# Performance work log

Measured on AMD Instinct MI355X. Metric: run time of the kernel, lower is better.

Reference implementation:

```python
import jax, jax.numpy as jnp
import numpy as np
import math

F_DIM = 256      # feature_dims
NHEADS = 4
KEY_D = 64
VAL_D = 64
ITERS = 6        # update_iters
N_ATOMS = 100000
N_BONDS = 200000
NEI = 6
ATOM_FDIM = 31
BOND_FDIM = 37   # 31 + 6
NEG_SLOPE = 0.1


def setup_inputs() -> dict:
    key = jax.random.key(0)
    ks = jax.random.split(key, 13)
    s = 0.05
    return {
        "fatoms": jax.random.normal(ks[0], (N_ATOMS, ATOM_FDIM), jnp.float32),
        "fbonds": jax.random.normal(ks[1], (N_BONDS, BOND_FDIM), jnp.float32),
        "agraph": jax.random.randint(ks[2], (N_ATOMS, NEI), 0, N_BONDS),
        "bgraph": jax.random.randint(ks[3], (N_BONDS, NEI), 0, N_BONDS),
        "lig_scope": jax.random.randint(ks[4], (64, 2), 0, N_ATOMS),
        "W_emb": jax.random.normal(ks[5], (BOND_FDIM, F_DIM), jnp.float32) * s,
        "b_emb": jnp.zeros((F_DIM,), jnp.float32),
        "Wq": jax.random.normal(ks[6], (F_DIM, NHEADS * KEY_D), jnp.float32) * s,
        "Wk": jax.random.normal(ks[7], (F_DIM, NHEADS * KEY_D), jnp.float32) * s,
        "Wv": jax.random.normal(ks[8], (F_DIM, NHEADS * VAL_D), jnp.float32) * s,
        "Wout": jax.random.normal(ks[9], (VAL_D, F_DIM), jnp.float32) * s,
        "W_last": jax.random.normal(ks[10], (ATOM_FDIM + F_DIM, F_DIM), jnp.float32) * s,
        "b_last": jnp.zeros((F_DIM,), jnp.float32),
    }


def reference(fatoms, fbonds, agraph, bgraph, lig_scope,
              W_emb, b_emb, Wq, Wk, Wv, Wout, W_last, b_last):
    # Bond embedding + initial message
    fbonds_input = fbonds @ W_emb + b_emb                      # [B, F]
    message = jax.nn.leaky_relu(fbonds_input, NEG_SLOPE)
    # index 0 is the padding bond -> masked out in attention
    nei_mask = jnp.where(bgraph != 0, 0.0, -1e7)[:, None, :]   # [B, 1, NEI]
    inv_sqrt_kd = 1.0 / math.sqrt(KEY_D)

    for _ in range(ITERS - 1):
        nei = message[bgraph]                                  # [B, NEI, F] gather
        q = (message @ Wq).reshape(N_BONDS, NHEADS, KEY_D)     # [B, H, K]
        k = (nei @ Wk).reshape(N_BONDS, NEI, NHEADS, KEY_D)    # [B, NEI, H, K]
        v = (nei @ Wv).reshape(N_BONDS, NEI, NHEADS, VAL_D)    # [B, NEI, H, V]
        scores = jnp.einsum('bhk,bnhk->bhn', q, k) * inv_sqrt_kd + nei_mask
        attn = jax.nn.softmax(scores, axis=-1)                 # [B, H, NEI]
        out = jnp.einsum('bhn,bnhv->bhv', attn, v)             # [B, H, V]
        out = out.mean(axis=1)                                 # mean over heads -> [B, V]
        message = jax.nn.leaky_relu(fbonds_input + out @ Wout, NEG_SLOPE)

    # Aggregate incoming bond messages per atom (index 0 acts as padding row)
    nei_sum = message[agraph].sum(axis=1)                      # [A, F]
    h = jnp.concatenate([fatoms, nei_sum], axis=-1) @ W_last + b_last
    return jax.nn.leaky_relu(h, NEG_SLOPE)
```

## Files before the change

kernel.cpp:

```cpp
#include <hip/hip_runtime.h>

#define N_ATOMS 100000
#define N_BONDS 200000
#define NEI 6
#define ITERS 6

#define MB_PAD 200064
#define MT_B 1563
#define MT_A 782
#define KL 320
#define KVSTRIDE 768
#define QSTR 260

typedef __bf16 bf16x8 __attribute__((ext_vector_type(8)));
typedef float f32x4 __attribute__((ext_vector_type(4)));

__device__ __forceinline__ float b2f(unsigned short u) {
  union { unsigned int i; float f; } x; x.i = ((unsigned int)u) << 16; return x.f;
}
__device__ __forceinline__ unsigned short f2b(float f) {
  union { float f; unsigned int i; } x; x.f = f;
  unsigned int r = (x.i + 0x7FFFu + ((x.i >> 16) & 1u)) >> 16;
  return (unsigned short)r;
}
__device__ __forceinline__ float lrelu(float v) { return v > 0.f ? v : 0.1f * v; }

#if defined(__has_builtin)
#  if __has_builtin(__builtin_amdgcn_cvt_f32_fp8) && __has_builtin(__builtin_amdgcn_cvt_pk_fp8_f32)
#    define HW_FP8 1
#  endif
#endif

__device__ __forceinline__ unsigned char f2e4m3_sw(float f) {
  union { float f; unsigned u; } x; x.f = f;
  unsigned s = (x.u >> 24) & 0x80u;
  unsigned ax = x.u & 0x7FFFFFFFu;
  if (ax >= 0x43E00000u) return (unsigned char)(s | 0x7Eu);
  if (ax < 0x3A800000u)  return (unsigned char)s;
  if (ax < 0x3C800000u) {
    union { unsigned u; float f; } a; a.u = ax;
    unsigned n = (unsigned)(a.f * 512.0f + 0.5f);
    return (unsigned char)(s | n);
  }
  unsigned r = ax + 0x0007FFFFu + ((ax >> 20) & 1u);
  unsigned e32 = r >> 23;
  unsigned mant = (r >> 20) & 7u;
  int e8 = (int)e32 - 120;
  if (e8 >= 16) return (unsigned char)(s | 0x7Eu);
  return (unsigned char)(s | ((unsigned)e8 << 3) | mant);
}
__device__ __forceinline__ float dec8_sw(unsigned b) {
  unsigned s = (b & 0x80u) << 24;
  unsigned e = (b >> 3) & 0xFu, m = b & 7u;
  if (e) { union { unsigned u; float f; } x; x.u = s | ((e + 120u) << 23) | (m << 20); return x.f; }
  float v = (float)m * 0.001953125f;
  return (b & 0x80u) ? -v : v;
}
#ifdef HW_FP8
__device__ __forceinline__ unsigned char f2e4m3(float f) {
  return (unsigned char)(__builtin_amdgcn_cvt_pk_fp8_f32(f, f, 0, false) & 0xFF);
}
#define DEC0(x) __builtin_amdgcn_cvt_f32_fp8((int)(x), 0)
#define DEC1(x) __builtin_amdgcn_cvt_f32_fp8((int)(x), 1)
#define DEC2(x) __builtin_amdgcn_cvt_f32_fp8((int)(x), 2)
#define DEC3(x) __builtin_amdgcn_cvt_f32_fp8((int)(x), 3)
#else
__device__ __forceinline__ unsigned char f2e4m3(float f) { return f2e4m3_sw(f); }
#define DEC0(x) dec8_sw((x) & 0xFFu)
#define DEC1(x) dec8_sw(((x) >> 8) & 0xFFu)
#define DEC2(x) dec8_sw(((x) >> 16) & 0xFFu)
#define DEC3(x) dec8_sw(((x) >> 24) & 0xFFu)
#endif

__global__ __launch_bounds__(256) void pack_weights(
    const float* __restrict__ Wq, const float* __restrict__ Wk,
    const float* __restrict__ Wv, const float* __restrict__ Wemb,
    const float* __restrict__ Wout, const float* __restrict__ Wlast,
    unsigned short* __restrict__ wkvT, unsigned short* __restrict__ wqT,
    unsigned short* __restrict__ wmsgT, unsigned short* __restrict__ wlastT)
{
  int t = blockIdx.x * 256 + threadIdx.x;
  {
    int n = t >> 8, k = t & 255;
    wkvT[t] = f2b((n < 256) ? Wk[k * 256 + n] : Wv[k * 256 + (n - 256)]);
  }
  if (t < 65536) {
    int n = t >> 8, k = t & 255;
    wqT[t] = f2b(Wq[k * 256 + n]);
  }
  if (t < 32768) {
    int n = t >> 7, k = t & 127;
    float v = 0.f;
    if (k < 64)       v = Wout[k * 256 + n];
    else if (k < 101) v = Wemb[(k - 64) * 256 + n];
    wmsgT[t] = f2b(v);
  }
  if (t < 256 * KL) {
    int n = t / KL, k = t % KL;
    float v = 0.f;
    if (k < 256)      v = Wlast[(31 + k) * 256 + n];
    else if (k < 287) v = Wlast[(k - 256) * 256 + n];
    wlastT[t] = f2b(v);
  }
}

__global__ __launch_bounds__(256) void pack_bonds(
    const float* __restrict__ fbonds, unsigned short* __restrict__ A2)
{
  int t = blockIdx.x * 256 + threadIdx.x;
  int r = t >> 7, c = t & 127;
  float v = 0.f;
  if (c >= 64 && c < 101 && r < N_BONDS) v = fbonds[r * 37 + (c - 64)];
  A2[t] = f2b(v);
}

template<int EP>
__global__ __launch_bounds__(256) void gemm_bt(
    const unsigned short* __restrict__ A,
    const unsigned short* __restrict__ BT,
    unsigned short* __restrict__ C0,
    float* __restrict__ Fout,
    const float* __restrict__ Xf,
    int K, int N, int Mreal)
{
  __shared__ __align__(16) unsigned short As[128 * 64];
  __shared__ __align__(16) unsigned short Bs[128 * 64];
  const int tid  = threadIdx.x;
  const int wave = tid >> 6, lane = tid & 63;
  const int wr = wave >> 1, wc = wave & 1;
  const int lhi = lane >> 4, llo = lane & 15;
  const int mBase = blockIdx.x * 128;
  const int nBase = blockIdx.y * 128;
  const int crow = tid >> 3, ccol = tid & 7;

  f32x4 acc[4][4];
  #pragma unroll
  for (int i = 0; i < 4; ++i)
    #pragma unroll
    for (int j = 0; j < 4; ++j)
      acc[i][j] = f32x4{0.f, 0.f, 0.f, 0.f};

  for (int k0 = 0; k0 < K; k0 += 64) {
    __syncthreads();
    #pragma unroll
    for (int r = 0; r < 4; ++r) {
      const unsigned short* ga =
          A + (size_t)(mBase + r * 32 + crow) * K + (k0 + ccol * 8);
      __builtin_amdgcn_global_load_lds(
          (const __attribute__((address_space(1))) void*)ga,
          (__attribute__((address_space(3))) void*)(As + r * 2048 + wave * 512), 16, 0, 0);
      const unsigned short* gb =
          BT + (size_t)(nBase + r * 32 + crow) * K + (k0 + ccol * 8);
      __builtin_amdgcn_global_load_lds(
          (const __attribute__((address_space(1))) void*)gb,
          (__attribute__((address_space(3))) void*)(Bs + r * 2048 + wave * 512), 16, 0, 0);
    }
    __syncthreads();
    #pragma unroll
    for (int ks = 0; ks < 2; ++ks) {
      bf16x8 af[4], bfv[4];
      #pragma unroll
      for (int i = 0; i < 4; ++i)
        af[i] = *reinterpret_cast<const bf16x8*>(&As[(wr * 64 + i * 16 + llo) * 64 + ks * 32 + lhi * 8]);
      #pragma unroll
      for (int j = 0; j < 4; ++j)
        bfv[j] = *reinterpret_cast<const bf16x8*>(&Bs[(wc * 64 + j * 16 + llo) * 64 + ks * 32 + lhi * 8]);
      #pragma unroll
      for (int i = 0; i < 4; ++i)
        #pragma unroll
        for (int j = 0; j < 4; ++j)
          acc[i][j] = __builtin_amdgcn_mfma_f32_16x16x32_bf16(af[i], bfv[j], acc[i][j], 0, 0, 0);
    }
  }

  #pragma unroll
  for (int i = 0; i < 4; ++i) {
    #pragma unroll
    for (int j = 0; j < 4; ++j) {
      const int col = nBase + wc * 64 + j * 16 + llo;
      #pragma unroll
      for (int r = 0; r < 4; ++r) {
        const int row = mBase + wr * 64 + i * 16 + lhi * 4 + r;
        const float v = acc[i][j][r];
        if (EP == 0) {
          C0[(size_t)row * N + col] = f2b(v);
        } else if (EP == 1) {
          C0[(size_t)row * N + col] = f2b(lrelu(v + Xf[col]));
        } else if (EP == 3) {
          if (row < Mreal) Fout[(size_t)row * N + col] = lrelu(v + Xf[col]);
        } else {
          unsigned char* kvb = (unsigned char*)C0;
          if (nBase < 256) {
            kvb[(size_t)row * KVSTRIDE + col] = f2e4m3(v);
          } else {
            *(unsigned short*)(kvb + (size_t)row * KVSTRIDE + 256 +
                               (size_t)(col - 256) * 2) = f2b(v);
          }
        }
      }
    }
  }
}

#define LOADSET(bn_, kd_, vu_, BL) do {                                        \
    const int wid_ = mBase + (BL);                                             \
    _Pragma("unroll")                                                          \
    for (int n = 0; n < NEI; ++n) bn_[n] = bgraph[(size_t)wid_ * NEI + n];     \
    _Pragma("unroll")                                                          \
    for (int n = 0; n < NEI; ++n) {                                            \
      const unsigned char* bp_ = kv + (size_t)bn_[n] * KVSTRIDE;               \
      kd_[n] = *reinterpret_cast<const unsigned*>(bp_ + lane * 4);             \
      vu_[n] = *reinterpret_cast<const ushort4*>(bp_ + 256 + lane * 8);        \
    }                                                                          \
  } while (0)

#define COMPUTEB(bn_, kd_, vu_, BL) do {                                       \
    const int wid_ = mBase + (BL);                                             \
    const ushort4 qu_ = *reinterpret_cast<const ushort4*>(                     \
        &smem[(size_t)(BL) * QSTR + lane * 4]);                                \
    const float q0_ = b2f(qu_.x), q1_ = b2f(qu_.y);                            \
    const float q2_ = b2f(qu_.z), q3_ = b2f(qu_.w);                            \
    float sc_[NEI];                                                            \
    _Pragma("unroll")                                                          \
    for (int n = 0; n < NEI; ++n) {                                            \
      float p_ = q0_ * DEC0(kd_[n]) + q1_ * DEC1(kd_[n]) +                     \
                 q2_ * DEC2(kd_[n]) + q3_ * DEC3(kd_[n]);                      \
      p_ += __shfl_xor(p_, 1); p_ += __shfl_xor(p_, 2);                        \
      p_ += __shfl_xor(p_, 4); p_ += __shfl_xor(p_, 8);                        \
      sc_[n] = p_ * SCL + (bn_[n] != 0 ? 0.f : -1e7f);                         \
    }                                                                          \
    const float m_ =                                                           \
        fmaxf(fmaxf(fmaxf(sc_[0], sc_[1]), fmaxf(sc_[2], sc_[3])),             \
              fmaxf(sc_[4], sc_[5]));                                          \
    float s_ = 0.f, o0_ = 0.f, o1_ = 0.f, o2_ = 0.f, o3_ = 0.f;                \
    _Pragma("unroll")                                                          \
    for (int n = 0; n < NEI; ++n) {                                            \
      const float e_ = exp2f(sc_[n] - m_);                                     \
      s_ += e_;                                                                \
      o0_ += e_ * b2f(vu_[n].x); o1_ += e_ * b2f(vu_[n].y);                    \
      o2_ += e_ * b2f(vu_[n].z); o3_ += e_ * b2f(vu_[n].w);                    \
    }                                                                          \
    const float inv_ = 0.25f * __builtin_amdgcn_rcpf(s_);                      \
    o0_ *= inv_; o1_ *= inv_; o2_ *= inv_; o3_ *= inv_;                        \
    o0_ += __shfl_xor(o0_, 16); o0_ += __shfl_xor(o0_, 32);                    \
    o1_ += __shfl_xor(o1_, 16); o1_ += __shfl_xor(o1_, 32);                    \
    o2_ += __shfl_xor(o2_, 16); o2_ += __shfl_xor(o2_, 32);                    \
    o3_ += __shfl_xor(o3_, 16); o3_ += __shfl_xor(o3_, 32);                    \
    if (lane < 16) {                                                           \
      ushort4 ov_;                                                             \
      ov_.x = f2b(o0_); ov_.y = f2b(o1_);                                      \
      ov_.z = f2b(o2_); ov_.w = f2b(o3_);                                      \
      *reinterpret_cast<ushort4*>(A2 + (size_t)wid_ * 128 + lane * 4) = ov_;   \
    }                                                                          \
  } while (0)

__global__ __launch_bounds__(512, 4) void fused_qattn(
    const unsigned short* __restrict__ msg,
    const unsigned short* __restrict__ wqT,
    const unsigned char* __restrict__ kv,
    const int* __restrict__ bgraph,
    unsigned short* __restrict__ A2)
{
  __shared__ __align__(16) unsigned short smem[128 * QSTR];
  const int tid  = threadIdx.x;
  const int wave = tid >> 6, lane = tid & 63;
  const int wr = wave >> 2, wc = wave & 3;
  const int lhi = lane >> 4, llo = lane & 15;
  const int mBase = blockIdx.x * 128;
  const int crow = tid >> 3, ccol = tid & 7;

  f32x4 acc[4][4];
  #pragma unroll
  for (int i = 0; i < 4; ++i)
    #pragma unroll
    for (int j = 0; j < 4; ++j)
      acc[i][j] = f32x4{0.f, 0.f, 0.f, 0.f};

  for (int k0 = 0; k0 < 256; k0 += 64) {
    __syncthreads();
    #pragma unroll
    for (int r = 0; r < 2; ++r) {
      const unsigned short* ga =
          msg + (size_t)(mBase + r * 64 + crow) * 256 + (k0 + ccol * 8);
      __builtin_amdgcn_global_load_lds(
          (const __attribute__((address_space(1))) void*)ga,
          (__attribute__((address_space(3))) void*)(smem + r * 4096 + wave * 512),
          16, 0, 0);
    }
    #pragma unroll
    for (int r = 0; r < 4; ++r) {
      const unsigned short* gb =
          wqT + (size_t)(r * 64 + crow) * 256 + (k0 + ccol * 8);
      __builtin_amdgcn_global_load_lds(
          (const __attribute__((address_space(1))) void*)gb,
          (__attribute__((address_space(3))) void*)(smem + 8192 + r * 4096 + wave * 512),
          16, 0, 0);
    }
    __syncthreads();
    #pragma unroll
    for (int ks = 0; ks < 2; ++ks) {
      bf16x8 af[4], bfv[4];
      #pragma unroll
      for (int i = 0; i < 4; ++i)
        af[i] = *reinterpret_cast<const bf16x8*>(
            &smem[(wr * 64 + i * 16 + llo) * 64 + ks * 32 + lhi * 8]);
      #pragma unroll
      for (int j = 0; j < 4; ++j)
        bfv[j] = *reinterpret_cast<const bf16x8*>(
            &smem[8192 + (wc * 64 + j * 16 + llo) * 64 + ks * 32 + lhi * 8]);
      #pragma unroll
      for (int i = 0; i < 4; ++i)
        #pragma unroll
        for (int j = 0; j < 4; ++j)
          acc[i][j] = __builtin_amdgcn_mfma_f32_16x16x32_bf16(af[i], bfv[j], acc[i][j], 0, 0, 0);
    }
  }
  __syncthreads();

  #pragma unroll
  for (int i = 0; i < 4; ++i) {
    #pragma unroll
    for (int j = 0; j < 4; ++j) {
      const int col = wc * 64 + j * 16 + llo;
      #pragma unroll
      for (int r = 0; r < 4; ++r) {
        const int row = wr * 64 + i * 16 + lhi * 4 + r;
        smem[row * QSTR + col] = f2b(acc[i][j][r]);
      }
    }
  }
  __syncthreads();

  const float SCL = 0.125f * 1.44269504089f;
  int bnA[NEI], bnB[NEI];
  unsigned kdA[NEI], kdB[NEI];
  ushort4 vuA[NEI], vuB[NEI];
  const int b0 = wave * 16;
  int nv = N_BONDS - (mBase + b0);
  if (nv > 16) nv = 16;
  if (nv > 0) {
    LOADSET(bnA, kdA, vuA, b0);
    #pragma unroll 1
    for (int it = 0; it < 16; it += 2) {
      if (it + 1 < nv) LOADSET(bnB, kdB, vuB, b0 + it + 1);
      if (it < nv)     COMPUTEB(bnA, kdA, vuA, b0 + it);
      if (it + 2 < nv) LOADSET(bnA, kdA, vuA, b0 + it + 2);
      if (it + 1 < nv) COMPUTEB(bnB, kdB, vuB, b0 + it + 1);
    }
  }
}

__global__ __launch_bounds__(256) void atom_gather(
    const unsigned short* __restrict__ msg,
    const int* __restrict__ agraph,
    const float* __restrict__ fatoms,
    unsigned short* __restrict__ apad)
{
  const int aid  = blockIdx.x * 4 + (threadIdx.x >> 6);
  const int lane = threadIdx.x & 63;
  if (aid >= N_ATOMS) return;
  float s0 = 0, s1 = 0, s2 = 0, s3 = 0;
  #pragma unroll
  for (int n = 0; n < NEI; ++n) {
    const int b = agraph[aid * NEI + n];
    const ushort4 u = *reinterpret_cast<const ushort4*>(msg + (size_t)b * 256 + lane * 4);
    s0 += b2f(u.x); s1 += b2f(u.y); s2 += b2f(u.z); s3 += b2f(u.w);
  }
  ushort4 ov; ov.x = f2b(s0); ov.y = f2b(s1); ov.z = f2b(s2); ov.w = f2b(s3);
  *reinterpret_cast<ushort4*>(apad + (size_t)aid * KL + lane * 4) = ov;
  apad[(size_t)aid * KL + 256 + lane] =
      (lane < 31) ? f2b(fatoms[(size_t)aid * 31 + lane]) : (unsigned short)0;
}

__global__ __launch_bounds__(256) void diag_out(float* out, int n, float code) {
  int t = blockIdx.x * 256 + threadIdx.x;
  if (t < n) out[t] = (t == 0) ? code : 0.f;
}

extern "C" void kernel_launch(void* const* d_in, const int* in_sizes, int n_in,
                              void* d_out, int out_size, void* d_ws, size_t ws_size,
                              hipStream_t stream) {
  const float* fatoms = (const float*)d_in[0];
  const float* fbonds = (const float*)d_in[1];
  const int* agraph   = (const int*)d_in[2];
  const int* bgraph   = (const int*)d_in[3];
  const float* Wemb   = (const float*)d_in[5];
  const float* bemb   = (const float*)d_in[6];
  const float* Wq     = (const float*)d_in[7];
  const float* Wk     = (const float*)d_in[8];
  const float* Wv     = (const float*)d_in[9];
  const float* Wout   = (const float*)d_in[10];
  const float* Wlast  = (const float*)d_in[11];
  const float* blast  = (const float*)d_in[12];
  float* out          = (float*)d_out;

  char* ws = (char*)d_ws;
  size_t off = 0;
  auto alloc = [&](size_t bytes) {
    char* p = ws + off; off += (bytes + 511) & ~(size_t)511; return p;
  };
  unsigned short* msg    = (unsigned short*)alloc((size_t)MB_PAD * 256 * 2);
  unsigned char*  kv     = (unsigned char*)alloc((size_t)MB_PAD * KVSTRIDE);
  unsigned short* A2     = (unsigned short*)alloc((size_t)MB_PAD * 128 * 2);
  unsigned short* wkvT   = (unsigned short*)alloc((size_t)512 * 256 * 2);
  unsigned short* wqT    = (unsigned short*)alloc((size_t)256 * 256 * 2);
  unsigned short* wmsgT  = (unsigned short*)alloc((size_t)256 * 128 * 2);
  unsigned short* wlastT = (unsigned short*)alloc((size_t)256 * KL * 2);
  unsigned short* apad   = (unsigned short*)kv;

  if (off > ws_size) {
    diag_out<<<dim3((out_size + 255) / 256), dim3(256), 0, stream>>>(
        out, out_size, 10000.f + (float)(ws_size >> 20));
    return;
  }

  pack_weights<<<dim3(512), dim3(256), 0, stream>>>(
      Wq, Wk, Wv, Wemb, Wout, Wlast, wkvT, wqT, wmsgT, wlastT);
  pack_bonds<<<dim3(MB_PAD * 128 / 256), dim3(256), 0, stream>>>(fbonds, A2);

  gemm_bt<1><<<dim3(MT_B, 2), dim3(256), 0, stream>>>(
      A2, wmsgT, msg, (float*)nullptr, bemb, 128, 256, MB_PAD);

  for (int it = 0; it < ITERS - 1; ++it) {
    gemm_bt<4><<<dim3(MT_B, 4), dim3(256), 0, stream>>>(
        msg, wkvT, (unsigned short*)kv, (float*)nullptr, (const float*)nullptr,
        256, 512, MB_PAD);
    fused_qattn<<<dim3(MT_B), dim3(512), 0, stream>>>(msg, wqT, kv, bgraph, A2);
    gemm_bt<1><<<dim3(MT_B, 2), dim3(256), 0, stream>>>(
        A2, wmsgT, msg, (float*)nullptr, bemb, 128, 256, MB_PAD);
  }

  atom_gather<<<dim3(N_ATOMS / 4), dim3(256), 0, stream>>>(msg, agraph, fatoms, apad);
  gemm_bt<3><<<dim3(MT_A, 2), dim3(256), 0, stream>>>(
      apad, wlastT, (unsigned short*)nullptr, out, blast, KL, 256, N_ATOMS);
}
```

Measured before the change: 2.149 ms.

## Halve fused attention tile, swizzle weight LDS layout, scalarize neighbor indices

The fused Q-projection plus attention kernel now handles 64 bonds per block instead of 128. This shrinks shared memory and accumulator registers and raises the launch bound to 8 blocks per CU, so more neighbor gathers are in flight at once. The transposed weights are stored with an XOR swizzle on K, and the GEMM B-fragment reads apply the matching swizzle to avoid LDS bank conflicts. Neighbor indices are also moved to scalar registers with readfirstlane, and a packed fp8 decode is used when available. The cost is twice as many blocks, each redoing the Wq tile load, plus extra register pressure risk from the higher occupancy target.

```diff
diff --git a/kernel.cpp b/kernel.cpp
--- a/kernel.cpp
+++ b/kernel.cpp
@@ -7,6 +7,7 @@
 
 #define MB_PAD 200064
 #define MT_B 1563
+#define MT_Q 3126
 #define MT_A 782
 #define KL 320
 #define KVSTRIDE 768
@@ -14,6 +15,7 @@
 
 typedef __bf16 bf16x8 __attribute__((ext_vector_type(8)));
 typedef float f32x4 __attribute__((ext_vector_type(4)));
+typedef float f32x2 __attribute__((ext_vector_type(2)));
 
 __device__ __forceinline__ float b2f(unsigned short u) {
   union { unsigned int i; float f; } x; x.i = ((unsigned int)u) << 16; return x.f;
@@ -28,6 +30,9 @@
 #if defined(__has_builtin)
 #  if __has_builtin(__builtin_amdgcn_cvt_f32_fp8) && __has_builtin(__builtin_amdgcn_cvt_pk_fp8_f32)
 #    define HW_FP8 1
+#  endif
+#  if __has_builtin(__builtin_amdgcn_cvt_pk_f32_fp8)
+#    define HW_PKFP8 1
 #  endif
 #endif
 
@@ -72,6 +77,10 @@
 #define DEC3(x) dec8_sw(((x) >> 24) & 0xFFu)
 #endif
 
+__device__ __forceinline__ int kswz(int k, int n) {
+  return (k & ~63) | ((k & 63) ^ ((n & 7) << 3));
+}
+
 __global__ __launch_bounds__(256) void pack_weights(
     const float* __restrict__ Wq, const float* __restrict__ Wk,
     const float* __restrict__ Wv, const float* __restrict__ Wemb,
@@ -82,25 +91,26 @@
   int t = blockIdx.x * 256 + threadIdx.x;
   {
     int n = t >> 8, k = t & 255;
-    wkvT[t] = f2b((n < 256) ? Wk[k * 256 + n] : Wv[k * 256 + (n - 256)]);
+    wkvT[n * 256 + kswz(k, n)] =
+        f2b((n < 256) ? Wk[k * 256 + n] : Wv[k * 256 + (n - 256)]);
   }
   if (t < 65536) {
     int n = t >> 8, k = t & 255;
-    wqT[t] = f2b(Wq[k * 256 + n]);
+    wqT[n * 256 + kswz(k, n)] = f2b(Wq[k * 256 + n]);
   }
   if (t < 32768) {
     int n = t >> 7, k = t & 127;
     float v = 0.f;
     if (k < 64)       v = Wout[k * 256 + n];
     else if (k < 101) v = Wemb[(k - 64) * 256 + n];
-    wmsgT[t] = f2b(v);
+    wmsgT[n * 128 + kswz(k, n)] = f2b(v);
   }
   if (t < 256 * KL) {
     int n = t / KL, k = t % KL;
     float v = 0.f;
     if (k < 256)      v = Wlast[(31 + k) * 256 + n];
     else if (k < 287) v = Wlast[(k - 256) * 256 + n];
-    wlastT[t] = f2b(v);
+    wlastT[n * KL + kswz(k, n)] = f2b(v);
   }
 }
 
@@ -164,7 +174,8 @@
         af[i] = *reinterpret_cast<const bf16x8*>(&As[(wr * 64 + i * 16 + llo) * 64 + ks * 32 + lhi * 8]);
       #pragma unroll
       for (int j = 0; j < 4; ++j)
-        bfv[j] = *reinterpret_cast<const bf16x8*>(&Bs[(wc * 64 + j * 16 + llo) * 64 + ks * 32 + lhi * 8]);
+        bfv[j] = *reinterpret_cast<const bf16x8*>(
+            &Bs[(wc * 64 + j * 16 + llo) * 64 + ((ks * 32 + lhi * 8) ^ ((llo & 7) << 3))]);
       #pragma unroll
       for (int i = 0; i < 4; ++i)
         #pragma unroll
@@ -202,29 +213,42 @@
   }
 }
 
-#define LOADSET(bn_, kd_, vu_, BL) do {                                        \
-    const int wid_ = mBase + (BL);                                             \
+#define PLOAD(bn_, kd_, vu_, BL) do {                                          \
+    const int uw_ = __builtin_amdgcn_readfirstlane(mBase + (BL));              \
     _Pragma("unroll")                                                          \
-    for (int n = 0; n < NEI; ++n) bn_[n] = bgraph[(size_t)wid_ * NEI + n];     \
+    for (int n = 0; n < NEI; ++n)                                              \
+      bn_[n] = __builtin_amdgcn_readfirstlane(bgraph[(size_t)uw_ * NEI + n]);  \
     _Pragma("unroll")                                                          \
     for (int n = 0; n < NEI; ++n) {                                            \
-      const unsigned char* bp_ = kv + (size_t)bn_[n] * KVSTRIDE;               \
+      const unsigned char* bp_ = kv + (size_t)(unsigned)bn_[n] * KVSTRIDE;     \
       kd_[n] = *reinterpret_cast<const unsigned*>(bp_ + lane * 4);             \
       vu_[n] = *reinterpret_cast<const ushort4*>(bp_ + 256 + lane * 8);        \
     }                                                                          \
   } while (0)
 
-#define COMPUTEB(bn_, kd_, vu_, BL) do {                                       \
-    const int wid_ = mBase + (BL);                                             \
+#ifdef HW_PKFP8
+#define QKDOT(p_, kd_) do {                                                    \
+    const f32x2 lo_ = __builtin_amdgcn_cvt_pk_f32_fp8((int)(kd_), false);      \
+    const f32x2 hi_ = __builtin_amdgcn_cvt_pk_f32_fp8((int)(kd_), true);       \
+    p_ = q0 * lo_.x + q1 * lo_.y + q2 * hi_.x + q3 * hi_.y;                    \
+  } while (0)
+#else
+#define QKDOT(p_, kd_) do {                                                    \
+    p_ = q0 * DEC0(kd_) + q1 * DEC1(kd_) + q2 * DEC2(kd_) + q3 * DEC3(kd_);    \
+  } while (0)
+#endif
+
+#define PCOMP(bn_, kd_, vu_, BL) do {                                          \
+    const int bl_ = (BL);                                                      \
     const ushort4 qu_ = *reinterpret_cast<const ushort4*>(                     \
-        &smem[(size_t)(BL) * QSTR + lane * 4]);                                \
-    const float q0_ = b2f(qu_.x), q1_ = b2f(qu_.y);                            \
-    const float q2_ = b2f(qu_.z), q3_ = b2f(qu_.w);                            \
+        &smem[bl_ * QSTR + lane * 4]);                                         \
+    const float q0 = b2f(qu_.x), q1 = b2f(qu_.y);                              \
+    const float q2 = b2f(qu_.z), q3 = b2f(qu_.w);                              \
     float sc_[NEI];                                                            \
     _Pragma("unroll")                                                          \
     for (int n = 0; n < NEI; ++n) {                                            \
-      float p_ = q0_ * DEC0(kd_[n]) + q1_ * DEC1(kd_[n]) +                     \
-                 q2_ * DEC2(kd_[n]) + q3_ * DEC3(kd_[n]);                      \
+      float p_;                                                                \
+      QKDOT(p_, kd_[n]);                                                       \
       p_ += __shfl_xor(p_, 1); p_ += __shfl_xor(p_, 2);                        \
       p_ += __shfl_xor(p_, 4); p_ += __shfl_xor(p_, 8);                        \
       sc_[n] = p_ * SCL + (bn_[n] != 0 ? 0.f : -1e7f);                         \
@@ -250,42 +274,41 @@
       ushort4 ov_;                                                             \
       ov_.x = f2b(o0_); ov_.y = f2b(o1_);                                      \
       ov_.z = f2b(o2_); ov_.w = f2b(o3_);                                      \
-      *reinterpret_cast<ushort4*>(A2 + (size_t)wid_ * 128 + lane * 4) = ov_;   \
+      *reinterpret_cast<ushort4*>(                                             \
+          A2 + (size_t)(mBase + bl_) * 128 + lane * 4) = ov_;                  \
     }                                                                          \
   } while (0)
 
-__global__ __launch_bounds__(512, 4) void fused_qattn(
+__global__ __launch_bounds__(512, 8) void fused_qattn(
     const unsigned short* __restrict__ msg,
     const unsigned short* __restrict__ wqT,
     const unsigned char* __restrict__ kv,
     const int* __restrict__ bgraph,
     unsigned short* __restrict__ A2)
 {
-  __shared__ __align__(16) unsigned short smem[128 * QSTR];
+  __shared__ __align__(16) unsigned short smem[20480];
   const int tid  = threadIdx.x;
   const int wave = tid >> 6, lane = tid & 63;
   const int wr = wave >> 2, wc = wave & 3;
   const int lhi = lane >> 4, llo = lane & 15;
-  const int mBase = blockIdx.x * 128;
+  const int mBase = blockIdx.x * 64;
   const int crow = tid >> 3, ccol = tid & 7;
 
-  f32x4 acc[4][4];
+  f32x4 acc[2][4];
   #pragma unroll
-  for (int i = 0; i < 4; ++i)
+  for (int i = 0; i < 2; ++i)
     #pragma unroll
     for (int j = 0; j < 4; ++j)
       acc[i][j] = f32x4{0.f, 0.f, 0.f, 0.f};
 
   for (int k0 = 0; k0 < 256; k0 += 64) {
     __syncthreads();
-    #pragma unroll
-    for (int r = 0; r < 2; ++r) {
+    {
       const unsigned short* ga =
-          msg + (size_t)(mBase + r * 64 + crow) * 256 + (k0 + ccol * 8);
+          msg + (size_t)(mBase + crow) * 256 + (k0 + ccol * 8);
       __builtin_amdgcn_global_load_lds(
           (const __attribute__((address_space(1))) void*)ga,
-          (__attribute__((address_space(3))) void*)(smem + r * 4096 + wave * 512),
-          16, 0, 0);
+          (__attribute__((address_space(3))) void*)(smem + wave * 512), 16, 0, 0);
     }
     #pragma unroll
     for (int r = 0; r < 4; ++r) {
@@ -293,23 +316,24 @@
           wqT + (size_t)(r * 64 + crow) * 256 + (k0 + ccol * 8);
       __builtin_amdgcn_global_load_lds(
           (const __attribute__((address_space(1))) void*)gb,
-          (__attribute__((address_space(3))) void*)(smem + 8192 + r * 4096 + wave * 512),
+          (__attribute__((address_space(3))) void*)(smem + 4096 + r * 4096 + wave * 512),
           16, 0, 0);
     }
     __syncthreads();
     #pragma unroll
     for (int ks = 0; ks < 2; ++ks) {
-      bf16x8 af[4], bfv[4];
-      #pragma unroll
-      for (int i = 0; i < 4; ++i)
+      bf16x8 af[2], bfv[4];
+      #pragma unroll
+      for (int i = 0; i < 2; ++i)
         af[i] = *reinterpret_cast<const bf16x8*>(
-            &smem[(wr * 64 + i * 16 + llo) * 64 + ks * 32 + lhi * 8]);
+            &smem[(wr * 32 + i * 16 + llo) * 64 + ks * 32 + lhi * 8]);
       #pragma unroll
       for (int j = 0; j < 4; ++j)
         bfv[j] = *reinterpret_cast<const bf16x8*>(
-            &smem[8192 + (wc * 64 + j * 16 + llo) * 64 + ks * 32 + lhi * 8]);
-      #pragma unroll
-      for (int i = 0; i < 4; ++i)
+            &smem[4096 + (wc * 64 + j * 16 + llo) * 64 +
+                  ((ks * 32 + lhi * 8) ^ ((llo & 7) << 3))]);
+      #pragma unroll
+      for (int i = 0; i < 2; ++i)
         #pragma unroll
         for (int j = 0; j < 4; ++j)
           acc[i][j] = __builtin_amdgcn_mfma_f32_16x16x32_bf16(af[i], bfv[j], acc[i][j], 0, 0, 0);
@@ -318,13 +342,13 @@
   __syncthreads();
 
   #pragma unroll
-  for (int i = 0; i < 4; ++i) {
+  for (int i = 0; i < 2; ++i) {
     #pragma unroll
     for (int j = 0; j < 4; ++j) {
       const int col = wc * 64 + j * 16 + llo;
       #pragma unroll
       for (int r = 0; r < 4; ++r) {
-        const int row = wr * 64 + i * 16 + lhi * 4 + r;
+        const int row = wr * 32 + i * 16 + lhi * 4 + r;
         smem[row * QSTR + col] = f2b(acc[i][j][r]);
       }
     }
@@ -332,20 +356,20 @@
   __syncthreads();
 
   const float SCL = 0.125f * 1.44269504089f;
-  int bnA[NEI], bnB[NEI];
-  unsigned kdA[NEI], kdB[NEI];
-  ushort4 vuA[NEI], vuB[NEI];
-  const int b0 = wave * 16;
+  const int b0 = wave * 8;
   int nv = N_BONDS - (mBase + b0);
-  if (nv > 16) nv = 16;
+  if (nv > 8) nv = 8;
   if (nv > 0) {
-    LOADSET(bnA, kdA, vuA, b0);
+    int bnA[NEI], bnB[NEI];
+    unsigned kdA[NEI], kdB[NEI];
+    ushort4 vuA[NEI], vuB[NEI];
+    PLOAD(bnA, kdA, vuA, b0);
     #pragma unroll 1
-    for (int it = 0; it < 16; it += 2) {
-      if (it + 1 < nv) LOADSET(bnB, kdB, vuB, b0 + it + 1);
-      if (it < nv)     COMPUTEB(bnA, kdA, vuA, b0 + it);
-      if (it + 2 < nv) LOADSET(bnA, kdA, vuA, b0 + it + 2);
-      if (it + 1 < nv) COMPUTEB(bnB, kdB, vuB, b0 + it + 1);
+    for (int it = 0; it < 8; it += 2) {
+      if (it + 1 < nv) PLOAD(bnB, kdB, vuB, b0 + it + 1);
+      if (it < nv)     PCOMP(bnA, kdA, vuA, b0 + it);
+      if (it + 2 < nv) PLOAD(bnA, kdA, vuA, b0 + it + 2);
+      if (it + 1 < nv) PCOMP(bnB, kdB, vuB, b0 + it + 1);
     }
   }
 }
@@ -425,7 +449,7 @@
     gemm_bt<4><<<dim3(MT_B, 4), dim3(256), 0, stream>>>(
         msg, wkvT, (unsigned short*)kv, (float*)nullptr, (const float*)nullptr,
         256, 512, MB_PAD);
-    fused_qattn<<<dim3(MT_B), dim3(512), 0, stream>>>(msg, wqT, kv, bgraph, A2);
+    fused_qattn<<<dim3(MT_Q), dim3(512), 0, stream>>>(msg, wqT, kv, bgraph, A2);
     gemm_bt<1><<<dim3(MT_B, 2), dim3(256), 0, stream>>>(
         A2, wmsgT, msg, (float*)nullptr, bemb, 128, 256, MB_PAD);
   }
```

After: 3.520 ms. 63.8% more time.
